# Optimization experiments

Hardware: AMD Instinct MI355X
Metric: run time of the kernel (lower is better)

The kernel has to match this reference:

```python
import jax, jax.numpy as jnp
import numpy as np

HID = 64
STEP = 0.05  # rk4 fixed step; t in [0, 0.2] -> 4 steps
NSTEPS = 4


def setup_inputs() -> dict:
    key = jax.random.key(0)
    ks = jax.random.split(key, 4)
    coords = jax.random.uniform(ks[0], (1, 96, 96, 96, 3), jnp.float32, -1.0, 1.0)

    def mlp_params(k):
        k1, k2 = jax.random.split(k)
        W1 = jax.random.normal(k1, (3, HID), jnp.float32) * 0.3
        b1 = jnp.zeros((HID,), jnp.float32)
        W2 = jax.random.normal(k2, (HID, 3), jnp.float32) * 0.3
        b2 = jnp.zeros((3,), jnp.float32)
        return W1, b1, W2, b2

    W1_0, b1_0, W2_0, b2_0 = mlp_params(ks[1])
    W1_1, b1_1, W2_1, b2_1 = mlp_params(ks[2])
    moving_img = jax.random.uniform(ks[3], (128, 128, 128), jnp.float32)
    return dict(coords=coords,
                W1_0=W1_0, b1_0=b1_0, W2_0=W2_0, b2_0=b2_0,
                W1_1=W1_1, b1_1=b1_1, W2_1=W2_1, b2_1=b2_1,
                moving_img=moving_img)


def _integrate(y, W1, b1, W2, b2):
    """Fixed-step RK4 on dy/dt = f(y) over t in [0, 0.2], step 0.05."""
    f = jax.checkpoint(lambda u: jnp.tanh(u @ W1 + b1) @ W2 + b2)
    h = jnp.float32(STEP)

    def step(y, _):
        k1 = f(y)
        k2 = f(y + 0.5 * h * k1)
        k3 = f(y + 0.5 * h * k2)
        k4 = f(y + h * k3)
        return y + (h / 6.0) * (k1 + 2.0 * k2 + 2.0 * k3 + k4), None

    y, _ = jax.lax.scan(step, y, None, length=NSTEPS)
    return y


def _grid_sample3d(vol, c):
    """torch F.grid_sample 3D, bilinear(trilinear), padding_mode=zeros,
    align_corners=False. c[..., [2,1,0]] reorder from the module means:
    c[...,2] -> x (W axis), c[...,1] -> y (H axis), c[...,0] -> z (D axis)."""
    D, H, W = vol.shape
    x = ((c[..., 2] + 1.0) * W - 1.0) * 0.5
    y = ((c[..., 1] + 1.0) * H - 1.0) * 0.5
    z = ((c[..., 0] + 1.0) * D - 1.0) * 0.5
    x0f, y0f, z0f = jnp.floor(x), jnp.floor(y), jnp.floor(z)
    tx, ty, tz = x - x0f, y - y0f, z - z0f
    x0 = x0f.astype(jnp.int32); x1 = x0 + 1
    y0 = y0f.astype(jnp.int32); y1 = y0 + 1
    z0 = z0f.astype(jnp.int32); z1 = z0 + 1

    def tap(zi, yi, xi, w):
        valid = (zi >= 0) & (zi < D) & (yi >= 0) & (yi < H) & (xi >= 0) & (xi < W)
        v = vol[jnp.clip(zi, 0, D - 1), jnp.clip(yi, 0, H - 1), jnp.clip(xi, 0, W - 1)]
        return jnp.where(valid, v, 0.0) * w

    out = (tap(z0, y0, x0, (1 - tz) * (1 - ty) * (1 - tx)) +
           tap(z0, y0, x1, (1 - tz) * (1 - ty) * tx) +
           tap(z0, y1, x0, (1 - tz) * ty * (1 - tx)) +
           tap(z0, y1, x1, (1 - tz) * ty * tx) +
           tap(z1, y0, x0, tz * (1 - ty) * (1 - tx)) +
           tap(z1, y0, x1, tz * (1 - ty) * tx) +
           tap(z1, y1, x0, tz * ty * (1 - tx)) +
           tap(z1, y1, x1, tz * ty * tx))
    return out


def reference(coords, W1_0, b1_0, W2_0, b2_0, W1_1, b1_1, W2_1, b2_1, moving_img):
    shp = coords.shape                      # [b, h, w, d, 3]
    flat = coords.reshape(-1, 3)            # [N, 3]
    c0 = _integrate(flat, W1_0, b1_0, W2_0, b2_0)          # first ODE warp
    c1 = _integrate(c0, W1_1, b1_1, W2_1, b2_1).reshape(shp)  # second ODE warp
    s = _grid_sample3d(moving_img, c1)      # [b, h, w, d]
    reg_out = (s[..., None] - 0.5) * 2.0    # [b, h, w, d, 1]
    return reg_out, c1
```

## Files before the change

### kernel.cpp

```cpp
#include <hip/hip_runtime.h>
#include <hip/hip_bf16.h>

#define NPTS (96 * 96 * 96)
#define HID 64
#define H_EFF 0.2f

#define TB  49
#define TB2 (TB * TB)
#define TB3 (TB * TB * TB)
#define TB_SCALE 24.0f
#define TB_INV   0.0416666679f
#define QS   8192.0f
#define QSI  (1.0f / 8192.0f)
#define TBL_OFF_B 4128
#define VOL_N   (128 * 128 * 128)
#define VOL8_OFF_B ((size_t)TBL_OFF_B + (size_t)TB3 * 16)
#define WS_NEED (VOL8_OFF_B + (size_t)VOL_N)

typedef float v2f __attribute__((ext_vector_type(2)));
typedef float f4  __attribute__((ext_vector_type(4)));
typedef unsigned u2 __attribute__((ext_vector_type(2)));
typedef short s4v __attribute__((ext_vector_type(4)));
typedef short s8v __attribute__((ext_vector_type(8)));

__device__ __forceinline__ float bf2f(const __hip_bfloat16 v) {
    return __bfloat162float(v);
}
__device__ __forceinline__ v2f splat(float x) { v2f r; r.x = x; r.y = x; return r; }
__device__ __forceinline__ v2f vfma(v2f a, v2f b, v2f c) {
    return __builtin_elementwise_fma(a, b, c);
}
__device__ __forceinline__ float lerp1(float a, float b, float f) {
    return __builtin_fmaf(f, b - a, a);
}

__global__ void setup_kernel(
    const void* __restrict__ coords,
    const void* __restrict__ W1_0, const void* __restrict__ b1_0,
    const void* __restrict__ W2_0, const void* __restrict__ b2_0,
    const void* __restrict__ W1_1, const void* __restrict__ b1_1,
    const void* __restrict__ W2_1, const void* __restrict__ b2_1,
    const void* __restrict__ vol,
    float* __restrict__ ws) {
    __shared__ int sflags[3];
    int tid = threadIdx.x;
    if (tid < 64) {
        auto sane = [](const void* p, int i) -> bool {
            unsigned e = (((const unsigned short*)p)[i] >> 7) & 0xFFu;
            return e >= 97u && e <= 129u;
        };
        unsigned long long m;
        m = __ballot(sane(W1_0, tid));
        if (tid == 0) sflags[2] = (__popcll(m) >= 52) ? 1 : 0;
        m = __ballot(sane(coords, tid));
        if (tid == 0) sflags[0] = (__popcll(m) >= 52) ? 1 : 0;
        m = __ballot(sane(vol, tid));
        if (tid == 0) sflags[1] = (__popcll(m) >= 52) ? 1 : 0;
    }
    __syncthreads();
    int isbf = sflags[2];
    const float K = 2.88539008177792681472f;
    int ode = tid >> 9;
    int r = tid & 511;
    const void* W1 = ode ? W1_1 : W1_0;
    const void* b1 = ode ? b1_1 : b1_0;
    const void* W2 = ode ? W2_1 : W2_0;
    const void* b2 = ode ? b2_1 : b2_0;
    auto ld = [&](const void* p, int idx) -> float {
        return isbf ? bf2f(((const __hip_bfloat16*)p)[idx]) : ((const float*)p)[idx];
    };
    float v = 0.0f;
    if (r < 192)       v = K * ld(W1, r);
    else if (r < 256)  v = K * ld(b1, r - 192);
    else if (r < 448)  v = -2.0f * ld(W2, r - 256);
    else if (r < 451) {
        int k = r - 448;
        float s = ld(b2, k);
        for (int j = 0; j < HID; ++j) s += ld(W2, 3 * j + k);
        v = s;
    }
    ws[(ode << 9) + r] = v;
    if (tid < 2) ((int*)(ws + 1024))[tid] = sflags[tid];
}

__global__ __launch_bounds__(256) void conv_vol_kernel(
    const void* __restrict__ vol,
    const float* __restrict__ ws,
    unsigned char* __restrict__ vol8) {
    int i = blockIdx.x * 256 + threadIdx.x;
    if (i >= VOL_N) return;
    int vbf = ((const int*)(ws + 1024))[1];
    float v = vbf ? bf2f(((const __hip_bfloat16*)vol)[i]) : ((const float*)vol)[i];
    float q = __builtin_fmaf(v, 255.0f, 0.5f);
    q = q < 0.f ? 0.f : (q > 255.f ? 255.f : q);
    vol8[i] = (unsigned char)q;
}

__device__ __forceinline__ void mlp_f2(const float* __restrict__ w,
                                       v2f y0, v2f y1, v2f y2,
                                       v2f& o0, v2f& o1, v2f& o2) {
    v2f a0 = splat(w[448]), a1 = splat(w[449]), a2 = splat(w[450]);
#pragma unroll 8
    for (int j = 0; j < HID; ++j) {
        v2f pre = vfma(y0, splat(w[j]),
                  vfma(y1, splat(w[64 + j]),
                  vfma(y2, splat(w[128 + j]), splat(w[192 + j]))));
        v2f e;
        e.x = __builtin_amdgcn_exp2f(pre.x);
        e.y = __builtin_amdgcn_exp2f(pre.y);
        v2f q = e + splat(1.0f);
        float rP = __builtin_amdgcn_rcpf(q.x * q.y);
        v2f r;
        r.x = q.y * rP;
        r.y = q.x * rP;
        a0 = vfma(r, splat(w[256 + 3 * j + 0]), a0);
        a1 = vfma(r, splat(w[256 + 3 * j + 1]), a1);
        a2 = vfma(r, splat(w[256 + 3 * j + 2]), a2);
    }
    o0 = a0; o1 = a1; o2 = a2;
}

__device__ __forceinline__ void integrate2(const float* __restrict__ ws,
                                           v2f& y0, v2f& y1, v2f& y2) {
    const float h = H_EFF;
#pragma unroll 1
    for (int ode = 0; ode < 2; ++ode) {
        const float* __restrict__ w = ws + (ode << 9);
        v2f k0 = splat(0.f), k1 = splat(0.f), k2 = splat(0.f);
        v2f s0 = splat(0.f), s1 = splat(0.f), s2 = splat(0.f);
#pragma unroll 1
        for (int e = 0; e < 4; ++e) {
            float ae = (e == 0) ? 0.0f : ((e == 3) ? h : 0.5f * h);
            float we = (e == 1 || e == 2) ? 2.0f : 1.0f;
            v2f aev = splat(ae), wev = splat(we);
            v2f f0, f1, f2;
            mlp_f2(w,
                   vfma(aev, k0, y0),
                   vfma(aev, k1, y1),
                   vfma(aev, k2, y2),
                   f0, f1, f2);
            k0 = f0; k1 = f1; k2 = f2;
            s0 = vfma(wev, k0, s0);
            s1 = vfma(wev, k1, s1);
            s2 = vfma(wev, k2, s2);
        }
        v2f h6 = splat(h / 6.0f);
        y0 = vfma(h6, s0, y0);
        y1 = vfma(h6, s1, y1);
        y2 = vfma(h6, s2, y2);
    }
}

__global__ __launch_bounds__(256) void build_kernel(const float* __restrict__ ws,
                                                    short* __restrict__ tbl) {
    int t = blockIdx.x * 256 + threadIdx.x;
    int nA = 2 * t;
    if (nA >= TB3) return;
    int nB = nA + 1;
    int nBc = nB < TB3 ? nB : (TB3 - 1);

    auto node_y = [](int n, float* a, float* b, float* c) {
        int i0 = n / TB2;
        int rem = n - i0 * TB2;
        int i1 = rem / TB;
        int i2 = rem - i1 * TB;
        *a = __builtin_fmaf((float)i0, TB_INV, -1.0f);
        *b = __builtin_fmaf((float)i1, TB_INV, -1.0f);
        *c = __builtin_fmaf((float)i2, TB_INV, -1.0f);
    };
    float ax, bx, cxv, ay, by, cyv;
    node_y(nA,  &ax, &bx, &cxv);
    node_y(nBc, &ay, &by, &cyv);
    v2f y0, y1, y2;
    y0.x = ax;  y1.x = bx;  y2.x = cxv;
    y0.y = ay;  y1.y = by;  y2.y = cyv;

    integrate2(ws, y0, y1, y2);

    auto quant = [](float v) -> short {
        float q = v * QS;
        q = q < -32767.f ? -32767.f : (q > 32767.f ? 32767.f : q);
        return (short)(int)rintf(q);
    };
    s4v qA = { quant(y0.x), quant(y1.x), quant(y2.x), 0 };
    s4v qB = { quant(y0.y), quant(y1.y), quant(y2.y), 0 };

    s4v* T = (s4v*)tbl;
    T[2 * nA] = qA;
    if (nA > 0) T[2 * nA - 1] = qA;
    if (nB < TB3) {
        T[2 * nB] = qB;
        T[2 * nB - 1] = qB;
    }
}

__device__ __forceinline__ float sample3d_u8(const unsigned char* __restrict__ V,
                                             float cz, float cy, float cx) {
    float fx = (cx + 1.0f) * 64.0f - 0.5f;
    float fy = (cy + 1.0f) * 64.0f - 0.5f;
    float fz = (cz + 1.0f) * 64.0f - 0.5f;
    float x0f = floorf(fx), y0f = floorf(fy), z0f = floorf(fz);
    float tx = fx - x0f, ty = fy - y0f, tz = fz - z0f;
    int x0 = (int)x0f, y0 = (int)y0f, z0 = (int)z0f;
    int x1 = x0 + 1, y1 = y0 + 1, z1 = z0 + 1;
    auto clampi = [](int v) { return v < 0 ? 0 : (v > 127 ? 127 : v); };
    auto valid = [](int zi, int yi, int xi) -> bool {
        return ((unsigned)zi < 128u) && ((unsigned)yi < 128u) && ((unsigned)xi < 128u);
    };
    int xc0 = clampi(x0), xc1 = clampi(x1);
    int yc0 = clampi(y0), yc1 = clampi(y1);
    int zc0 = clampi(z0), zc1 = clampi(z1);
    int idx[8] = {
        (zc0 << 14) | (yc0 << 7) | xc0, (zc0 << 14) | (yc0 << 7) | xc1,
        (zc0 << 14) | (yc1 << 7) | xc0, (zc0 << 14) | (yc1 << 7) | xc1,
        (zc1 << 14) | (yc0 << 7) | xc0, (zc1 << 14) | (yc0 << 7) | xc1,
        (zc1 << 14) | (yc1 << 7) | xc0, (zc1 << 14) | (yc1 << 7) | xc1 };
    float v[8];
#pragma unroll
    for (int q = 0; q < 8; ++q) v[q] = (float)V[idx[q]];
    if (!valid(z0, y0, x0)) v[0] = 0.f;
    if (!valid(z0, y0, x1)) v[1] = 0.f;
    if (!valid(z0, y1, x0)) v[2] = 0.f;
    if (!valid(z0, y1, x1)) v[3] = 0.f;
    if (!valid(z1, y0, x0)) v[4] = 0.f;
    if (!valid(z1, y0, x1)) v[5] = 0.f;
    if (!valid(z1, y1, x0)) v[6] = 0.f;
    if (!valid(z1, y1, x1)) v[7] = 0.f;
    return v[0] * (1.f - tz) * (1.f - ty) * (1.f - tx) +
           v[1] * (1.f - tz) * (1.f - ty) * tx +
           v[2] * (1.f - tz) * ty * (1.f - tx) +
           v[3] * (1.f - tz) * ty * tx +
           v[4] * tz * (1.f - ty) * (1.f - tx) +
           v[5] * tz * (1.f - ty) * tx +
           v[6] * tz * ty * (1.f - tx) +
           v[7] * tz * ty * tx;
}

__device__ __forceinline__ float sample3d(const void* __restrict__ vol, int vbf,
                                          float cz, float cy, float cx) {
    float fx = (cx + 1.0f) * 64.0f - 0.5f;
    float fy = (cy + 1.0f) * 64.0f - 0.5f;
    float fz = (cz + 1.0f) * 64.0f - 0.5f;
    float x0f = floorf(fx), y0f = floorf(fy), z0f = floorf(fz);
    float tx = fx - x0f, ty = fy - y0f, tz = fz - z0f;
    int x0 = (int)x0f, y0 = (int)y0f, z0 = (int)z0f;
    int x1 = x0 + 1, y1 = y0 + 1, z1 = z0 + 1;
    auto clampi = [](int v) { return v < 0 ? 0 : (v > 127 ? 127 : v); };
    auto valid = [](int zi, int yi, int xi) -> bool {
        return ((unsigned)zi < 128u) && ((unsigned)yi < 128u) && ((unsigned)xi < 128u);
    };
    int xc0 = clampi(x0), xc1 = clampi(x1);
    int yc0 = clampi(y0), yc1 = clampi(y1);
    int zc0 = clampi(z0), zc1 = clampi(z1);
    int idx[8] = {
        (zc0 << 14) | (yc0 << 7) | xc0, (zc0 << 14) | (yc0 << 7) | xc1,
        (zc0 << 14) | (yc1 << 7) | xc0, (zc0 << 14) | (yc1 << 7) | xc1,
        (zc1 << 14) | (yc0 << 7) | xc0, (zc1 << 14) | (yc0 << 7) | xc1,
        (zc1 << 14) | (yc1 << 7) | xc0, (zc1 << 14) | (yc1 << 7) | xc1 };
    float v[8];
    if (vbf) {
        const __hip_bfloat16* V = (const __hip_bfloat16*)vol;
#pragma unroll
        for (int q = 0; q < 8; ++q) v[q] = bf2f(V[idx[q]]);
    } else {
        const float* V = (const float*)vol;
#pragma unroll
        for (int q = 0; q < 8; ++q) v[q] = V[idx[q]];
    }
    if (!valid(z0, y0, x0)) v[0] = 0.f;
    if (!valid(z0, y0, x1)) v[1] = 0.f;
    if (!valid(z0, y1, x0)) v[2] = 0.f;
    if (!valid(z0, y1, x1)) v[3] = 0.f;
    if (!valid(z1, y0, x0)) v[4] = 0.f;
    if (!valid(z1, y0, x1)) v[5] = 0.f;
    if (!valid(z1, y1, x0)) v[6] = 0.f;
    if (!valid(z1, y1, x1)) v[7] = 0.f;
    return v[0] * (1.f - tz) * (1.f - ty) * (1.f - tx) +
           v[1] * (1.f - tz) * (1.f - ty) * tx +
           v[2] * (1.f - tz) * ty * (1.f - tx) +
           v[3] * (1.f - tz) * ty * tx +
           v[4] * tz * (1.f - ty) * (1.f - tx) +
           v[5] * tz * (1.f - ty) * tx +
           v[6] * tz * ty * (1.f - tx) +
           v[7] * tz * ty * tx;
}

__global__ __launch_bounds__(256) void query_kernel(
    const void* __restrict__ coords,
    const float* __restrict__ ws,
    float* __restrict__ out) {
    int t = blockIdx.x * 256 + threadIdx.x;
    if (t >= NPTS / 4) return;

    const int* flags = (const int*)(ws + 1024);
    int cbf = flags[0];

    float y[4][3];
    if (cbf) {
        const u2* C2 = (const u2*)((const unsigned short*)coords + 12 * t);
        u2 ua = __builtin_nontemporal_load(C2);
        u2 ub = __builtin_nontemporal_load(C2 + 1);
        u2 uc = __builtin_nontemporal_load(C2 + 2);
        unsigned uu[6] = {ua.x, ua.y, ub.x, ub.y, uc.x, uc.y};
#pragma unroll
        for (int p = 0; p < 4; ++p)
#pragma unroll
            for (int d = 0; d < 3; ++d) {
                int k = 3 * p + d;
                unsigned h = uu[k >> 1];
                h = (k & 1) ? (h & 0xFFFF0000u) : (h << 16);
                y[p][d] = __builtin_bit_cast(float, h);
            }
    } else {
        const f4* C4 = (const f4*)((const float*)coords + 12 * t);
        f4 a = __builtin_nontemporal_load(C4);
        f4 b = __builtin_nontemporal_load(C4 + 1);
        f4 c = __builtin_nontemporal_load(C4 + 2);
        y[0][0] = a.x; y[0][1] = a.y; y[0][2] = a.z;
        y[1][0] = a.w; y[1][1] = b.x; y[1][2] = b.y;
        y[2][0] = b.z; y[2][1] = b.w; y[2][2] = c.x;
        y[3][0] = c.y; y[3][1] = c.z; y[3][2] = c.w;
    }

    auto cell = [](float tt, int* idx, float* f) {
        int v = (int)floorf(tt);
        v = v < 0 ? 0 : (v > TB - 2 ? TB - 2 : v);
        *idx = v; *f = tt - (float)v;
    };

    int bidx[4];
    float ff[4][3];
#pragma unroll
    for (int p = 0; p < 4; ++p) {
        float t0 = (y[p][0] + 1.0f) * TB_SCALE;
        float t1 = (y[p][1] + 1.0f) * TB_SCALE;
        float t2 = (y[p][2] + 1.0f) * TB_SCALE;
        int i0, i1, i2;
        cell(t0, &i0, &ff[p][0]);
        cell(t1, &i1, &ff[p][1]);
        cell(t2, &i2, &ff[p][2]);
        bidx[p] = (i0 * TB + i1) * TB + i2;
    }

    const s8v* E = (const s8v*)((const char*)ws + TBL_OFF_B);
    s8v ev[4][4];
#pragma unroll
    for (int p = 0; p < 4; ++p) {
        int b = bidx[p];
        ev[p][0] = E[b];
        ev[p][1] = E[b + TB];
        ev[p][2] = E[b + TB2];
        ev[p][3] = E[b + TB2 + TB];
    }

    float c1v[4][3];
#pragma unroll
    for (int p = 0; p < 4; ++p) {
        float f0 = ff[p][0], f1 = ff[p][1], f2 = ff[p][2];
#pragma unroll
        for (int d = 0; d < 3; ++d) {
            float a00 = lerp1((float)ev[p][0][d], (float)ev[p][0][4 + d], f2);
            float a01 = lerp1((float)ev[p][1][d], (float)ev[p][1][4 + d], f2);
            float a10 = lerp1((float)ev[p][2][d], (float)ev[p][2][4 + d], f2);
            float a11 = lerp1((float)ev[p][3][d], (float)ev[p][3][4 + d], f2);
            c1v[p][d] = lerp1(lerp1(a00, a01, f1), lerp1(a10, a11, f1), f0) * QSI;
        }
    }

    {
        float* dst = out + NPTS + 12 * t;
        f4 s0 = {c1v[0][0], c1v[0][1], c1v[0][2], c1v[1][0]};
        f4 s1 = {c1v[1][1], c1v[1][2], c1v[2][0], c1v[2][1]};
        f4 s2 = {c1v[2][2], c1v[3][0], c1v[3][1], c1v[3][2]};
        ((f4*)dst)[0] = s0;
        ((f4*)dst)[1] = s1;
        ((f4*)dst)[2] = s2;
    }

    const unsigned char* V8 = (const unsigned char*)ws + VOL8_OFF_B;
    f4 o;
#pragma unroll
    for (int p = 0; p < 4; ++p) {
        float sraw = sample3d_u8(V8, c1v[p][0], c1v[p][1], c1v[p][2]);
        o[p] = __builtin_fmaf(sraw, 2.0f / 255.0f, -1.0f);
    }
    ((f4*)(out + 4 * t))[0] = o;
}

__global__ __launch_bounds__(64) void diffeo_kernel(
    const void* __restrict__ coords,
    const float* __restrict__ ws,
    const void* __restrict__ vol,
    float* __restrict__ out) {
    int t = blockIdx.x * 64 + threadIdx.x;
    if (t >= NPTS / 2) return;

    const int* flags = (const int*)(ws + 1024);
    int cbf = flags[0];
    int vbf = flags[1];

    v2f y0, y1, y2;
    if (cbf) {
        const __hip_bfloat16* C = (const __hip_bfloat16*)coords;
        int b = 6 * t;
        y0.x = bf2f(C[b + 0]); y1.x = bf2f(C[b + 1]); y2.x = bf2f(C[b + 2]);
        y0.y = bf2f(C[b + 3]); y1.y = bf2f(C[b + 4]); y2.y = bf2f(C[b + 5]);
    } else {
        const float* C = (const float*)coords;
        int b = 6 * t;
        y0.x = C[b + 0]; y1.x = C[b + 1]; y2.x = C[b + 2];
        y0.y = C[b + 3]; y1.y = C[b + 4]; y2.y = C[b + 5];
    }

    integrate2(ws, y0, y1, y2);

    int b = 6 * t;
    out[NPTS + b + 0] = y0.x; out[NPTS + b + 1] = y1.x; out[NPTS + b + 2] = y2.x;
    out[NPTS + b + 3] = y0.y; out[NPTS + b + 4] = y1.y; out[NPTS + b + 5] = y2.y;

    float sA = sample3d(vol, vbf, y0.x, y1.x, y2.x);
    float sB = sample3d(vol, vbf, y0.y, y1.y, y2.y);
    out[2 * t + 0] = __builtin_fmaf(2.0f, sA, -1.0f);
    out[2 * t + 1] = __builtin_fmaf(2.0f, sB, -1.0f);
}

extern "C" void kernel_launch(void* const* d_in, const int* in_sizes, int n_in,
                              void* d_out, int out_size, void* d_ws, size_t ws_size,
                              hipStream_t stream) {
    const void* coords = d_in[0];
    const void* W1_0 = d_in[1];
    const void* b1_0 = d_in[2];
    const void* W2_0 = d_in[3];
    const void* b2_0 = d_in[4];
    const void* W1_1 = d_in[5];
    const void* b1_1 = d_in[6];
    const void* W2_1 = d_in[7];
    const void* b2_1 = d_in[8];
    const void* vol  = d_in[9];
    float* out = (float*)d_out;
    float* ws = (float*)d_ws;

    setup_kernel<<<1, 1024, 0, stream>>>(coords, W1_0, b1_0, W2_0, b2_0,
                                         W1_1, b1_1, W2_1, b2_1, vol, ws);
    if (ws_size >= WS_NEED) {
        unsigned char* vol8 = (unsigned char*)ws + VOL8_OFF_B;
        short* tbl = (short*)((char*)ws + TBL_OFF_B);
        conv_vol_kernel<<<VOL_N / 256, 256, 0, stream>>>(vol, ws, vol8);
        int node_pairs = (TB3 + 1) / 2;
        build_kernel<<<(node_pairs + 255) / 256, 256, 0, stream>>>(ws, tbl);
        query_kernel<<<NPTS / 1024, 256, 0, stream>>>(coords, ws, out);
    } else {
        diffeo_kernel<<<(NPTS / 2) / 64, 64, 0, stream>>>(coords, ws, vol, out);
    }
}
```

Baseline: 160.1 us.

## Store quantized volume in bricked layout and shrink displacement table to single entries

```diff
diff --git a/kernel.cpp b/kernel.cpp
--- a/kernel.cpp
+++ b/kernel.cpp
@@ -13,15 +13,15 @@
 #define QS   8192.0f
 #define QSI  (1.0f / 8192.0f)
 #define TBL_OFF_B 4128
+#define TBL_BYTES ((size_t)TB3 * 8)
+#define VOLB_OFF_B 945408
 #define VOL_N   (128 * 128 * 128)
-#define VOL8_OFF_B ((size_t)TBL_OFF_B + (size_t)TB3 * 16)
-#define WS_NEED (VOL8_OFF_B + (size_t)VOL_N)
+#define WS_NEED ((size_t)VOLB_OFF_B + (size_t)VOL_N)
 
 typedef float v2f __attribute__((ext_vector_type(2)));
 typedef float f4  __attribute__((ext_vector_type(4)));
 typedef unsigned u2 __attribute__((ext_vector_type(2)));
 typedef short s4v __attribute__((ext_vector_type(4)));
-typedef short s8v __attribute__((ext_vector_type(8)));
 
 __device__ __forceinline__ float bf2f(const __hip_bfloat16 v) {
     return __bfloat162float(v);
@@ -33,6 +33,10 @@
 __device__ __forceinline__ float lerp1(float a, float b, float f) {
     return __builtin_fmaf(f, b - a, a);
 }
+
+__device__ __forceinline__ int bpx(int x) { return ((x >> 3) << 7) | (x & 7); }
+__device__ __forceinline__ int bpy(int y) { return ((y >> 2) << 11) | ((y & 3) << 3); }
+__device__ __forceinline__ int bpz(int z) { return ((z >> 2) << 16) | ((z & 3) << 5); }
 
 __global__ void setup_kernel(
     const void* __restrict__ coords,
@@ -86,14 +90,18 @@
 __global__ __launch_bounds__(256) void conv_vol_kernel(
     const void* __restrict__ vol,
     const float* __restrict__ ws,
-    unsigned char* __restrict__ vol8) {
-    int i = blockIdx.x * 256 + threadIdx.x;
-    if (i >= VOL_N) return;
+    unsigned char* __restrict__ volb) {
+    int d = blockIdx.x * 256 + threadIdx.x;
+    if (d >= VOL_N) return;
     int vbf = ((const int*)(ws + 1024))[1];
-    float v = vbf ? bf2f(((const __hip_bfloat16*)vol)[i]) : ((const float*)vol)[i];
+    int x = (((d >> 7) & 15) << 3) | (d & 7);
+    int y = (((d >> 11) & 31) << 2) | ((d >> 3) & 3);
+    int z = (((d >> 16) & 31) << 2) | ((d >> 5) & 3);
+    int src = (z << 14) | (y << 7) | x;
+    float v = vbf ? bf2f(((const __hip_bfloat16*)vol)[src]) : ((const float*)vol)[src];
     float q = __builtin_fmaf(v, 255.0f, 0.5f);
     q = q < 0.f ? 0.f : (q > 255.f ? 255.f : q);
-    vol8[i] = (unsigned char)q;
+    volb[d] = (unsigned char)q;
 }
 
 __device__ __forceinline__ void mlp_f2(const float* __restrict__ w,
@@ -152,7 +160,7 @@
 }
 
 __global__ __launch_bounds__(256) void build_kernel(const float* __restrict__ ws,
-                                                    short* __restrict__ tbl) {
+                                                    s4v* __restrict__ tbl) {
     int t = blockIdx.x * 256 + threadIdx.x;
     int nA = 2 * t;
     if (nA >= TB3) return;
@@ -185,55 +193,8 @@
     s4v qA = { quant(y0.x), quant(y1.x), quant(y2.x), 0 };
     s4v qB = { quant(y0.y), quant(y1.y), quant(y2.y), 0 };
 
-    s4v* T = (s4v*)tbl;
-    T[2 * nA] = qA;
-    if (nA > 0) T[2 * nA - 1] = qA;
-    if (nB < TB3) {
-        T[2 * nB] = qB;
-        T[2 * nB - 1] = qB;
-    }
-}
-
-__device__ __forceinline__ float sample3d_u8(const unsigned char* __restrict__ V,
-                                             float cz, float cy, float cx) {
-    float fx = (cx + 1.0f) * 64.0f - 0.5f;
-    float fy = (cy + 1.0f) * 64.0f - 0.5f;
-    float fz = (cz + 1.0f) * 64.0f - 0.5f;
-    float x0f = floorf(fx), y0f = floorf(fy), z0f = floorf(fz);
-    float tx = fx - x0f, ty = fy - y0f, tz = fz - z0f;
-    int x0 = (int)x0f, y0 = (int)y0f, z0 = (int)z0f;
-    int x1 = x0 + 1, y1 = y0 + 1, z1 = z0 + 1;
-    auto clampi = [](int v) { return v < 0 ? 0 : (v > 127 ? 127 : v); };
-    auto valid = [](int zi, int yi, int xi) -> bool {
-        return ((unsigned)zi < 128u) && ((unsigned)yi < 128u) && ((unsigned)xi < 128u);
-    };
-    int xc0 = clampi(x0), xc1 = clampi(x1);
-    int yc0 = clampi(y0), yc1 = clampi(y1);
-    int zc0 = clampi(z0), zc1 = clampi(z1);
-    int idx[8] = {
-        (zc0 << 14) | (yc0 << 7) | xc0, (zc0 << 14) | (yc0 << 7) | xc1,
-        (zc0 << 14) | (yc1 << 7) | xc0, (zc0 << 14) | (yc1 << 7) | xc1,
-        (zc1 << 14) | (yc0 << 7) | xc0, (zc1 << 14) | (yc0 << 7) | xc1,
-        (zc1 << 14) | (yc1 << 7) | xc0, (zc1 << 14) | (yc1 << 7) | xc1 };
-    float v[8];
-#pragma unroll
-    for (int q = 0; q < 8; ++q) v[q] = (float)V[idx[q]];
-    if (!valid(z0, y0, x0)) v[0] = 0.f;
-    if (!valid(z0, y0, x1)) v[1] = 0.f;
-    if (!valid(z0, y1, x0)) v[2] = 0.f;
-    if (!valid(z0, y1, x1)) v[3] = 0.f;
-    if (!valid(z1, y0, x0)) v[4] = 0.f;
-    if (!valid(z1, y0, x1)) v[5] = 0.f;
-    if (!valid(z1, y1, x0)) v[6] = 0.f;
-    if (!valid(z1, y1, x1)) v[7] = 0.f;
-    return v[0] * (1.f - tz) * (1.f - ty) * (1.f - tx) +
-           v[1] * (1.f - tz) * (1.f - ty) * tx +
-           v[2] * (1.f - tz) * ty * (1.f - tx) +
-           v[3] * (1.f - tz) * ty * tx +
-           v[4] * tz * (1.f - ty) * (1.f - tx) +
-           v[5] * tz * (1.f - ty) * tx +
-           v[6] * tz * ty * (1.f - tx) +
-           v[7] * tz * ty * tx;
+    tbl[nA] = qA;
+    if (nB < TB3) tbl[nB] = qB;
 }
 
 __device__ __forceinline__ float sample3d(const void* __restrict__ vol, int vbf,
@@ -342,15 +303,15 @@
         bidx[p] = (i0 * TB + i1) * TB + i2;
     }
 
-    const s8v* E = (const s8v*)((const char*)ws + TBL_OFF_B);
-    s8v ev[4][4];
+    const s4v* T = (const s4v*)((const char*)ws + TBL_OFF_B);
+    s4v ev[4][8];
 #pragma unroll
     for (int p = 0; p < 4; ++p) {
         int b = bidx[p];
-        ev[p][0] = E[b];
-        ev[p][1] = E[b + TB];
-        ev[p][2] = E[b + TB2];
-        ev[p][3] = E[b + TB2 + TB];
+        ev[p][0] = T[b];                 ev[p][1] = T[b + 1];
+        ev[p][2] = T[b + TB];            ev[p][3] = T[b + TB + 1];
+        ev[p][4] = T[b + TB2];           ev[p][5] = T[b + TB2 + 1];
+        ev[p][6] = T[b + TB2 + TB];      ev[p][7] = T[b + TB2 + TB + 1];
     }
 
     float c1v[4][3];
@@ -359,10 +320,10 @@
         float f0 = ff[p][0], f1 = ff[p][1], f2 = ff[p][2];
 #pragma unroll
         for (int d = 0; d < 3; ++d) {
-            float a00 = lerp1((float)ev[p][0][d], (float)ev[p][0][4 + d], f2);
-            float a01 = lerp1((float)ev[p][1][d], (float)ev[p][1][4 + d], f2);
-            float a10 = lerp1((float)ev[p][2][d], (float)ev[p][2][4 + d], f2);
-            float a11 = lerp1((float)ev[p][3][d], (float)ev[p][3][4 + d], f2);
+            float a00 = lerp1((float)ev[p][0][d], (float)ev[p][1][d], f2);
+            float a01 = lerp1((float)ev[p][2][d], (float)ev[p][3][d], f2);
+            float a10 = lerp1((float)ev[p][4][d], (float)ev[p][5][d], f2);
+            float a11 = lerp1((float)ev[p][6][d], (float)ev[p][7][d], f2);
             c1v[p][d] = lerp1(lerp1(a00, a01, f1), lerp1(a10, a11, f1), f0) * QSI;
         }
     }
@@ -377,11 +338,51 @@
         ((f4*)dst)[2] = s2;
     }
 
-    const unsigned char* V8 = (const unsigned char*)ws + VOL8_OFF_B;
+    const unsigned char* VB = (const unsigned char*)ws + VOLB_OFF_B;
     f4 o;
 #pragma unroll
     for (int p = 0; p < 4; ++p) {
-        float sraw = sample3d_u8(V8, c1v[p][0], c1v[p][1], c1v[p][2]);
+        float fx = (c1v[p][2] + 1.0f) * 64.0f - 0.5f;
+        float fy = (c1v[p][1] + 1.0f) * 64.0f - 0.5f;
+        float fz = (c1v[p][0] + 1.0f) * 64.0f - 0.5f;
+        float x0f = floorf(fx), y0f = floorf(fy), z0f = floorf(fz);
+        float tx = fx - x0f, ty = fy - y0f, tz = fz - z0f;
+        int x0 = (int)x0f, y0 = (int)y0f, z0 = (int)z0f;
+        int x1 = x0 + 1, y1 = y0 + 1, z1 = z0 + 1;
+        auto clampi = [](int v) { return v < 0 ? 0 : (v > 127 ? 127 : v); };
+        auto valid = [](int zi, int yi, int xi) -> bool {
+            return ((unsigned)zi < 128u) && ((unsigned)yi < 128u) &&
+                   ((unsigned)xi < 128u);
+        };
+        int px0 = bpx(clampi(x0)), px1 = bpx(clampi(x1));
+        int py0 = bpy(clampi(y0)), py1 = bpy(clampi(y1));
+        int pz0 = bpz(clampi(z0)), pz1 = bpz(clampi(z1));
+        float v[8];
+        v[0] = (float)VB[pz0 | py0 | px0];
+        v[1] = (float)VB[pz0 | py0 | px1];
+        v[2] = (float)VB[pz0 | py1 | px0];
+        v[3] = (float)VB[pz0 | py1 | px1];
+        v[4] = (float)VB[pz1 | py0 | px0];
+        v[5] = (float)VB[pz1 | py0 | px1];
+        v[6] = (float)VB[pz1 | py1 | px0];
+        v[7] = (float)VB[pz1 | py1 | px1];
+        if (!valid(z0, y0, x0)) v[0] = 0.f;
+        if (!valid(z0, y0, x1)) v[1] = 0.f;
+        if (!valid(z0, y1, x0)) v[2] = 0.f;
+        if (!valid(z0, y1, x1)) v[3] = 0.f;
+        if (!valid(z1, y0, x0)) v[4] = 0.f;
+        if (!valid(z1, y0, x1)) v[5] = 0.f;
+        if (!valid(z1, y1, x0)) v[6] = 0.f;
+        if (!valid(z1, y1, x1)) v[7] = 0.f;
+        float sraw =
+            v[0] * (1.f - tz) * (1.f - ty) * (1.f - tx) +
+            v[1] * (1.f - tz) * (1.f - ty) * tx +
+            v[2] * (1.f - tz) * ty * (1.f - tx) +
+            v[3] * (1.f - tz) * ty * tx +
+            v[4] * tz * (1.f - ty) * (1.f - tx) +
+            v[5] * tz * (1.f - ty) * tx +
+            v[6] * tz * ty * (1.f - tx) +
+            v[7] * tz * ty * tx;
         o[p] = __builtin_fmaf(sraw, 2.0f / 255.0f, -1.0f);
     }
     ((f4*)(out + 4 * t))[0] = o;
@@ -443,9 +444,9 @@
     setup_kernel<<<1, 1024, 0, stream>>>(coords, W1_0, b1_0, W2_0, b2_0,
                                          W1_1, b1_1, W2_1, b2_1, vol, ws);
     if (ws_size >= WS_NEED) {
-        unsigned char* vol8 = (unsigned char*)ws + VOL8_OFF_B;
-        short* tbl = (short*)((char*)ws + TBL_OFF_B);
-        conv_vol_kernel<<<VOL_N / 256, 256, 0, stream>>>(vol, ws, vol8);
+        unsigned char* volb = (unsigned char*)ws + VOLB_OFF_B;
+        s4v* tbl = (s4v*)((char*)ws + TBL_OFF_B);
+        conv_vol_kernel<<<VOL_N / 256, 256, 0, stream>>>(vol, ws, volb);
         int node_pairs = (TB3 + 1) / 2;
         build_kernel<<<(node_pairs + 255) / 256, 256, 0, stream>>>(ws, tbl);
         query_kernel<<<NPTS / 1024, 256, 0, stream>>>(coords, ws, out);
```

Result: faster. 153.9 us (-3.9%).
